# Optimization experiments

Hardware: AMD Instinct MI355X
Metric: run time of the kernel (lower is better)

Reference implementation:

```python
import jax, jax.numpy as jnp
import numpy as np

N, E, T, B, H, V, D = 100000, 400000, 20, 128, 400, 5000, 20


def setup_inputs() -> dict:
    key = jax.random.key(0)
    ks = iter(jax.random.split(key, 64))

    def ri(shape, hi):
        return jax.random.randint(next(ks), shape, 0, hi, dtype=jnp.int32)

    def rn(shape):
        return jax.random.normal(next(ks), shape, dtype=jnp.float32) * 0.05

    inp = {}
    for g in ("pd", "ast", "cf"):
        inp[f"x_{g}"] = ri((N, T), V)            # 20 token ids per node
        inp[f"ei_{g}"] = ri((2, E), N)            # [src; dst]
        inp[f"b_{g}"] = jnp.sort(ri((N,), B))     # graph assignment per node
        inp[f"emb_{g}"] = rn((V, D))
        inp[f"w_{g}"] = rn((3, H, H))             # per-step message weight
        inp[f"wih_{g}"] = rn((H, 3 * H))          # GRUCell input weights (r,z,n)
        inp[f"bih_{g}"] = jnp.zeros((3 * H,), jnp.float32)
        inp[f"whh_{g}"] = rn((H, 3 * H))
        inp[f"bhh_{g}"] = jnp.zeros((3 * H,), jnp.float32)
    for nm, (a, b) in zip(("1", "2", "21", "22", "3", "4"),
                          ((1200, 1000), (1000, 750), (750, 500), (500, 400), (400, 100), (100, 4))):
        inp[f"wl{nm}"] = rn((a, b))
        inp[f"bl{nm}"] = jnp.zeros((b,), jnp.float32)
    return inp


def _gru(m, h, wih, bih, whh, bhh):
    gi = m @ wih + bih
    gh = h @ whh + bhh
    ir, iz, inn = jnp.split(gi, 3, axis=-1)
    hr, hz, hn = jnp.split(gh, 3, axis=-1)
    r = jax.nn.sigmoid(ir + hr)
    z = jax.nn.sigmoid(iz + hz)
    n = jnp.tanh(inn + r * hn)
    return (1.0 - z) * n + z * h


def _ggc(h, ei, w, wih, bih, whh, bhh):
    # GatedGraphConv(H, num_layers=3): message = h @ w[i], scatter-add src->dst, GRU update
    src, dst = ei[0], ei[1]
    n_nodes = h.shape[0]
    for i in range(3):
        m = h @ w[i]                                   # [N, H]
        agg = jax.ops.segment_sum(m[src], dst, num_segments=n_nodes)  # [N, H]
        h = _gru(agg, h, wih, bih, whh, bhh)
    return h


def _branch(x, ei, b, emb, w, wih, bih, whh, bhh):
    h = emb[x].reshape(x.shape[0], -1)                 # [N, T*D] = [N, 400]
    h = jax.nn.relu(_ggc(h, ei, w, wih, bih, whh, bhh))
    pooled = jax.ops.segment_max(h, b, num_segments=B, indices_are_sorted=True)
    return jnp.where(jnp.isfinite(pooled), pooled, 0.0)  # guard empty segments


def reference(x_pd, ei_pd, b_pd, emb_pd, w_pd, wih_pd, bih_pd, whh_pd, bhh_pd,
              x_ast, ei_ast, b_ast, emb_ast, w_ast, wih_ast, bih_ast, whh_ast, bhh_ast,
              x_cf, ei_cf, b_cf, emb_cf, w_cf, wih_cf, bih_cf, whh_cf, bhh_cf,
              wl1, bl1, wl2, bl2, wl21, bl21, wl22, bl22, wl3, bl3, wl4, bl4):
    x1 = _branch(x_pd, ei_pd, b_pd, emb_pd, w_pd, wih_pd, bih_pd, whh_pd, bhh_pd)
    x2 = _branch(x_ast, ei_ast, b_ast, emb_ast, w_ast, wih_ast, bih_ast, whh_ast, bhh_ast)
    x4 = _branch(x_cf, ei_cf, b_cf, emb_cf, w_cf, wih_cf, bih_cf, whh_cf, bhh_cf)
    x = jnp.concatenate([x1, x2, x4], axis=1)          # [B, 1200]
    for wl, bl in ((wl1, bl1), (wl2, bl2), (wl21, bl21), (wl22, bl22), (wl3, bl3), (wl4, bl4)):
        x = jax.nn.relu(x @ wl + bl)                   # dropout inactive in eval mode
    return x
```

## Files before the change

### kernel.cpp

```cpp
#include <hip/hip_runtime.h>

typedef unsigned short u16;
typedef unsigned int u32;
typedef unsigned long long u64;
typedef float f32x4 __attribute__((ext_vector_type(4)));
typedef __bf16 bf16x8 __attribute__((ext_vector_type(8)));

#define KPAD 416
#define SWZ(r) ((((u32)(r)) & 3u) ^ ((((u32)(r)) >> 2) & 3u))

__device__ __forceinline__ float bf2f(u16 v){
  u32 x = ((u32)v) << 16; float f; __builtin_memcpy(&f, &x, 4); return f;
}
__device__ __forceinline__ u16 f2bf(float f){
  u32 x; __builtin_memcpy(&x, &f, 4);
  x += 0x7fffu + ((x >> 16) & 1u);
  return (u16)(x >> 16);
}
__device__ __forceinline__ void gll16(const u16* g, void* l){
  __builtin_amdgcn_global_load_lds(
      (const __attribute__((address_space(1))) u32*)(const void*)g,
      (__attribute__((address_space(3))) u32*)l, 16, 0, 0);
}
__device__ __forceinline__ int xcd_remap(int orig, int nwg){
  int q = nwg >> 3, r = nwg & 7;
  int xcd = orig & 7, idx = orig >> 3;
  return (xcd < r ? xcd * (q + 1) : r * (q + 1) + (xcd - r) * q) + idx;
}

__global__ void embed_k(const int* __restrict__ x, const float* __restrict__ emb,
                        u16* __restrict__ H, int N){
  int tid = blockIdx.x * 256 + threadIdx.x;
  if (tid >= N * 104) return;
  int n = tid / 104, cg = tid % 104, c = cg * 4;
  u16 r0 = 0, r1 = 0, r2 = 0, r3 = 0;
  if (c < 400){
    int t = c / 20, d = c % 20;
    int tok = x[n * 20 + t];
    f32x4 v = *(const f32x4*)(emb + (size_t)tok * 20 + d);
    r0 = f2bf(v[0]); r1 = f2bf(v[1]); r2 = f2bf(v[2]); r3 = f2bf(v[3]);
  }
  u64 pack = (u64)r0 | ((u64)r1 << 16) | ((u64)r2 << 32) | ((u64)r3 << 48);
  *(u64*)(H + (size_t)n * KPAD + c) = pack;
}

__global__ void convw_k(const float* __restrict__ src, u16* __restrict__ dst,
                        int srccols, int nout){
  int tid = blockIdx.x * 256 + threadIdx.x;
  if (tid >= nout * KPAD) return;
  int k = tid % KPAD, n = tid / KPAD;
  dst[tid] = (k < 400) ? f2bf(src[(size_t)k * srccols + n]) : (u16)0;
}

__global__ void pad_w(const float* __restrict__ src, u16* __restrict__ dst, int rows){
  int tid = blockIdx.x * 256 + threadIdx.x;
  if (tid >= rows * KPAD) return;
  int k = tid / KPAD, c = tid % KPAD;
  dst[tid] = (c < 400) ? f2bf(src[(size_t)k * 400 + c]) : (u16)0;
}

__global__ void count_k(const int* __restrict__ ei, int* __restrict__ cnt, int E){
  int t = blockIdx.x * 256 + threadIdx.x; if (t >= E) return;
  atomicAdd(&cnt[ei[E + t] + 1], 1);
}
__global__ void scan_blk(int* __restrict__ data, int* __restrict__ bsum, int total){
  __shared__ int sm[1024];
  int gid = blockIdx.x * 1024 + threadIdx.x;
  sm[threadIdx.x] = (gid < total) ? data[gid] : 0;
  __syncthreads();
  for (int off = 1; off < 1024; off <<= 1){
    int add = (threadIdx.x >= off) ? sm[threadIdx.x - off] : 0;
    __syncthreads();
    sm[threadIdx.x] += add;
    __syncthreads();
  }
  if (gid < total) data[gid] = sm[threadIdx.x];
  if (threadIdx.x == 1023 && bsum) bsum[blockIdx.x] = sm[1023];
}
__global__ void scan_add(int* __restrict__ data, const int* __restrict__ bsum, int total){
  int gid = blockIdx.x * 256 + threadIdx.x;
  if (gid >= total) return;
  int b = gid >> 10;
  if (b > 0) data[gid] += bsum[b - 1];
}
__global__ void copy_k(const int* __restrict__ s, int* __restrict__ d, int n){
  int t = blockIdx.x * 256 + threadIdx.x; if (t < n) d[t] = s[t];
}
__global__ void fill_k(const int* __restrict__ ei, int* __restrict__ cur,
                       int* __restrict__ srcl, int E){
  int t = blockIdx.x * 256 + threadIdx.x; if (t >= E) return;
  int d = ei[E + t];
  int p = atomicAdd(&cur[d], 1);
  srcl[p] = ei[t];
}
__global__ void bound_k(const int* __restrict__ bseg, int* __restrict__ segs, int N){
  int t = threadIdx.x; if (t > 128) return;
  int lo = 0, hi = N;
  while (lo < hi){ int mid = (lo + hi) >> 1; if (bseg[mid] < t) lo = mid + 1; else hi = mid; }
  segs[t] = lo;
}

__global__ void seg_sum(const int* __restrict__ offs, const int* __restrict__ srcl,
                        const u32* __restrict__ Mv, u32* __restrict__ Agg, int N){
  int n = blockIdx.x * 4 + (threadIdx.x >> 6);
  int lane = threadIdx.x & 63;
  if (n >= N || lane >= 52) return;
  int s = offs[n], e = offs[n + 1];
  float a[8] = {0.f,0.f,0.f,0.f,0.f,0.f,0.f,0.f};
  for (int i = s; i < e; i++){
    int sr = srcl[i];
    const u32* p = Mv + (size_t)sr * 208 + lane * 4;
    u32 v0 = p[0], v1 = p[1], v2 = p[2], v3 = p[3];
    a[0] += bf2f((u16)(v0 & 0xffffu)); a[1] += bf2f((u16)(v0 >> 16));
    a[2] += bf2f((u16)(v1 & 0xffffu)); a[3] += bf2f((u16)(v1 >> 16));
    a[4] += bf2f((u16)(v2 & 0xffffu)); a[5] += bf2f((u16)(v2 >> 16));
    a[6] += bf2f((u16)(v3 & 0xffffu)); a[7] += bf2f((u16)(v3 >> 16));
  }
  u32* q = Agg + (size_t)n * 208 + lane * 4;
  q[0] = (u32)f2bf(a[0]) | ((u32)f2bf(a[1]) << 16);
  q[1] = (u32)f2bf(a[2]) | ((u32)f2bf(a[3]) << 16);
  q[2] = (u32)f2bf(a[4]) | ((u32)f2bf(a[5]) << 16);
  q[3] = (u32)f2bf(a[6]) | ((u32)f2bf(a[7]) << 16);
}

__launch_bounds__(256, 2)
__global__ void gemm_msg(const u16* __restrict__ A, const u16* __restrict__ BT,
                         u16* __restrict__ C, int M, int nwg){
  __shared__ __align__(16) u16 smem[2][192 * 32];
  const int tid = threadIdx.x, lane = tid & 63, wave = tid >> 6;
  const int wg = xcd_remap(blockIdx.x, nwg);
  const int m0 = (wg / 7) * 128, n0 = (wg % 7) * 64;

  const u16* gsrc[3]; u32 ldo[3];
#pragma unroll
  for (int i = 0; i < 2; i++){
    u32 o = (u32)(wave * 2 + i) * 1024 + (u32)lane * 16;
    u32 r = o >> 6, cch = (o >> 4) & 3;
    int grow = m0 + (int)r; if (grow > M - 1) grow = M - 1;
    gsrc[i] = A + (size_t)grow * KPAD + ((cch ^ SWZ(r)) << 3);
    ldo[i] = o;
  }
  {
    u32 o = (u32)wave * 1024 + (u32)lane * 16;
    u32 r = o >> 6, cch = (o >> 4) & 3;
    int gn = n0 + (int)r; if (gn > 399) gn = 399;
    gsrc[2] = BT + (size_t)gn * KPAD + ((cch ^ SWZ(r)) << 3);
    ldo[2] = 8192 + o;
  }
  auto stage = [&](int p, int ks){
#pragma unroll
    for (int i = 0; i < 3; i++)
      gll16(gsrc[i] + ks * 32, (char*)smem + (size_t)p * 12288 + ldo[i]);
  };

  const int g = lane >> 4, rl = lane & 15;
  const int ar0 = wave * 32 + rl, ar1 = ar0 + 16;
  const u32 aoff0 = (u32)ar0 * 64 + ((g ^ SWZ(ar0)) << 4);
  const u32 aoff1 = (u32)ar1 * 64 + ((g ^ SWZ(ar1)) << 4);
  u32 boff[4];
#pragma unroll
  for (int j = 0; j < 4; j++){
    int br = j * 16 + rl;
    boff[j] = 8192u + (u32)br * 64 + ((g ^ SWZ(br)) << 4);
  }

  f32x4 zero = {0.f, 0.f, 0.f, 0.f};
  f32x4 acc[2][4];
#pragma unroll
  for (int i = 0; i < 2; i++)
#pragma unroll
    for (int j = 0; j < 4; j++) acc[i][j] = zero;

  stage(0, 0);
  __syncthreads();
  int cur = 0;
  for (int ks = 0; ks < 13; ks++){
    if (ks < 12) stage(cur ^ 1, ks + 1);
    const char* sb = (const char*)smem + (size_t)cur * 12288;
    bf16x8 a0 = *(const bf16x8*)(sb + aoff0);
    bf16x8 a1 = *(const bf16x8*)(sb + aoff1);
#pragma unroll
    for (int j = 0; j < 4; j++){
      bf16x8 bb = *(const bf16x8*)(sb + boff[j]);
      acc[0][j] = __builtin_amdgcn_mfma_f32_16x16x32_bf16(a0, bb, acc[0][j], 0, 0, 0);
      acc[1][j] = __builtin_amdgcn_mfma_f32_16x16x32_bf16(a1, bb, acc[1][j], 0, 0, 0);
    }
    __syncthreads();
    cur ^= 1;
  }

  const int rsub = (lane >> 4) * 4;
#pragma unroll
  for (int i = 0; i < 2; i++){
#pragma unroll
    for (int j = 0; j < 4; j++){
      int col = n0 + j * 16 + rl;
      if (col >= KPAD) continue;
#pragma unroll
      for (int r = 0; r < 4; r++){
        int row = m0 + wave * 32 + i * 16 + rsub + r;
        if (row >= M) continue;
        C[(size_t)row * KPAD + col] = (col < 400) ? f2bf(acc[i][j][r]) : (u16)0;
      }
    }
  }
}

__launch_bounds__(256, 2)
__global__ void gemm_gru(const u16* __restrict__ AG, const u16* __restrict__ AH,
                         const u16* __restrict__ WCT, const u16* __restrict__ WHHT,
                         const float* __restrict__ bih, const float* __restrict__ bhh,
                         u16* __restrict__ Out, int M, int nwg){
  __shared__ __align__(16) u16 lB[2][6144];
  const int tid = threadIdx.x, lane = tid & 63, wave = tid >> 6;
  const int wg = xcd_remap(blockIdx.x, nwg);
  const int m0 = (wg / 13) * 128, c0 = (wg % 13) * 32;

  const u16* gsrcB[3]; u32 ldoB[3];
#pragma unroll
  for (int ii = 0; ii < 3; ii++){
    int id = wave * 3 + ii;
    int tile = id >> 1, half = id & 1;
    const u16* Wsrc = (tile < 3) ? WCT : WHHT;
    int s = (tile < 3) ? tile : tile - 3;
    u32 o = (u32)half * 1024 + (u32)lane * 16;
    u32 r = o >> 6, cch = (o >> 4) & 3;
    int ncol = c0 + (int)r; if (ncol > 399) ncol = 399;
    gsrcB[ii] = Wsrc + (size_t)(s * 400 + ncol) * KPAD + ((cch ^ SWZ(r)) << 3);
    ldoB[ii] = (u32)tile * 2048 + o;
  }
  auto stageB = [&](int p, int ks){
#pragma unroll
    for (int ii = 0; ii < 3; ii++)
      gll16(gsrcB[ii] + ks * 32, (char*)(&lB[0][0]) + (size_t)p * 12288 + ldoB[ii]);
  };

  const int g = lane >> 4, rl = lane & 15;
  int rr0 = m0 + wave * 32 + rl;      if (rr0 > M - 1) rr0 = M - 1;
  int rr1 = m0 + wave * 32 + 16 + rl; if (rr1 > M - 1) rr1 = M - 1;
  const u16* pAG0 = AG + (size_t)rr0 * KPAD + g * 8;
  const u16* pAG1 = AG + (size_t)rr1 * KPAD + g * 8;
  const u16* pAH0 = AH + (size_t)rr0 * KPAD + g * 8;
  const u16* pAH1 = AH + (size_t)rr1 * KPAD + g * 8;

  u32 boffj[2];
#pragma unroll
  for (int j = 0; j < 2; j++){
    int br = j * 16 + rl;
    boffj[j] = (u32)br * 64 + ((g ^ SWZ(br)) << 4);
  }

  f32x4 zero = {0.f, 0.f, 0.f, 0.f};
  f32x4 acc[6][2][2];
#pragma unroll
  for (int t = 0; t < 6; t++)
#pragma unroll
    for (int i = 0; i < 2; i++)
#pragma unroll
      for (int j = 0; j < 2; j++) acc[t][i][j] = zero;

  bf16x8 aX[4], aY[4];
  auto loadA = [&](bf16x8 (&d)[4], int ks){
    d[0] = *(const bf16x8*)(pAG0 + ks * 32);
    d[1] = *(const bf16x8*)(pAG1 + ks * 32);
    d[2] = *(const bf16x8*)(pAH0 + ks * 32);
    d[3] = *(const bf16x8*)(pAH1 + ks * 32);
  };
  int cur = 0;
  auto body = [&](bf16x8 (&ac)[4], bf16x8 (&an)[4], int ks){
    if (ks < 12){ loadA(an, ks + 1); stageB(cur ^ 1, ks + 1); }
    const char* sb = (const char*)(&lB[0][0]) + (size_t)cur * 12288;
#pragma unroll
    for (int t = 0; t < 6; t++){
      bf16x8 b0 = *(const bf16x8*)(sb + t * 2048 + boffj[0]);
      bf16x8 b1 = *(const bf16x8*)(sb + t * 2048 + boffj[1]);
      bf16x8 x0 = (t < 3) ? ac[0] : ac[2];
      bf16x8 x1 = (t < 3) ? ac[1] : ac[3];
      acc[t][0][0] = __builtin_amdgcn_mfma_f32_16x16x32_bf16(x0, b0, acc[t][0][0], 0, 0, 0);
      acc[t][0][1] = __builtin_amdgcn_mfma_f32_16x16x32_bf16(x0, b1, acc[t][0][1], 0, 0, 0);
      acc[t][1][0] = __builtin_amdgcn_mfma_f32_16x16x32_bf16(x1, b0, acc[t][1][0], 0, 0, 0);
      acc[t][1][1] = __builtin_amdgcn_mfma_f32_16x16x32_bf16(x1, b1, acc[t][1][1], 0, 0, 0);
    }
    __syncthreads();
    cur ^= 1;
  };
  loadA(aX, 0);
  stageB(0, 0);
  __syncthreads();
#pragma unroll
  for (int kk = 0; kk < 6; kk++){
    body(aX, aY, 2 * kk);
    body(aY, aX, 2 * kk + 1);
  }
  body(aX, aY, 12);

  const int rsub = (lane >> 4) * 4;
#pragma unroll
  for (int j = 0; j < 2; j++){
    int col = c0 + j * 16 + rl;
    bool valid = col < 400;
    float bir = 0, biz = 0, bin = 0, bhr = 0, bhz = 0, bhn = 0;
    if (valid){
      bir = bih[col]; biz = bih[400 + col]; bin = bih[800 + col];
      bhr = bhh[col]; bhz = bhh[400 + col]; bhn = bhh[800 + col];
    }
#pragma unroll
    for (int i = 0; i < 2; i++){
#pragma unroll
      for (int r = 0; r < 4; r++){
        int row = m0 + wave * 32 + i * 16 + rsub + r;
        if (row >= M) continue;
        u16 outv = 0;
        if (valid){
          float ir = acc[0][i][j][r] + bir, iz = acc[1][i][j][r] + biz, inn = acc[2][i][j][r] + bin;
          float hr = acc[3][i][j][r] + bhr, hz = acc[4][i][j][r] + bhz, hn = acc[5][i][j][r] + bhn;
          float rg = 1.f / (1.f + __expf(-(ir + hr)));
          float zg = 1.f / (1.f + __expf(-(iz + hz)));
          float nx = inn + rg * hn;
          float tn = 1.f - 2.f / (1.f + __expf(2.f * nx));
          float hp = bf2f(AH[(size_t)row * KPAD + col]);
          float hv = (1.f - zg) * tn + zg * hp;
          outv = f2bf(hv);
        }
        Out[(size_t)row * KPAD + col] = outv;
      }
    }
  }
}

__global__ void pool_max(const u16* __restrict__ H, const int* __restrict__ segs,
                         u32* __restrict__ pooled, int goff){
  int b = blockIdx.x;
  int c = blockIdx.y * 256 + threadIdx.x;
  if (c >= 400) return;
  int s = segs[b], e = segs[b + 1], len = e - s;
  int chunk = blockIdx.z;
  int cs = s + (int)((long long)len * chunk / 4);
  int ce = s + (int)((long long)len * (chunk + 1) / 4);
  float mx = 0.f;
  for (int n = cs; n < ce; n++) mx = fmaxf(mx, bf2f(H[(size_t)n * KPAD + c]));
  if (mx > 0.f){
    u32 bits; __builtin_memcpy(&bits, &mx, 4);
    atomicMax(&pooled[b * 1200 + goff + c], bits);
  }
}

__global__ void wt_k(const float* __restrict__ src, float* __restrict__ dst,
                     int K, int Nout){
  int t = blockIdx.x * 256 + threadIdx.x;
  if (t >= K * Nout) return;
  int n = t / K, k = t % K;
  dst[t] = src[(size_t)k * Nout + n];
}
__global__ void mlp_dot(const float* __restrict__ A, const float* __restrict__ WT,
                        const float* __restrict__ bias, float* __restrict__ out,
                        int K, int Nout){
  int gw = (int)((blockIdx.x * 256u + threadIdx.x) >> 6);
  int lane = threadIdx.x & 63;
  if (gw >= 128 * Nout) return;
  int m = gw / Nout, n = gw % Nout;
  const float* a = A + (size_t)m * K;
  const float* w = WT + (size_t)n * K;
  float acc = 0.f;
  for (int k = lane; k < K; k += 64) acc = fmaf(a[k], w[k], acc);
#pragma unroll
  for (int off = 32; off; off >>= 1) acc += __shfl_xor(acc, off);
  if (lane == 0) out[(size_t)m * Nout + n] = fmaxf(acc + bias[n], 0.f);
}

extern "C" void kernel_launch(void* const* d_in, const int* in_sizes, int n_in,
                              void* d_out, int out_size, void* d_ws, size_t ws_size,
                              hipStream_t stream){
  const int N = in_sizes[2];
  const int E = in_sizes[1] / 2;

  char* base = (char*)d_ws;
  size_t off = 0;
  auto alloc = [&](size_t sz) -> char* {
    char* r = base + off;
    off += (sz + 255) & ~(size_t)255;
    return r;
  };
  u16* hA    = (u16*)alloc((size_t)N * KPAD * 2);
  u16* hB    = (u16*)alloc((size_t)N * KPAD * 2);
  u16* hC    = (u16*)alloc((size_t)N * KPAD * 2);
  u16* wcT   = (u16*)alloc((size_t)3 * 1200 * KPAD * 2);
  u16* whhT  = (u16*)alloc((size_t)1200 * KPAD * 2);
  u16* wihT  = (u16*)alloc((size_t)1200 * KPAD * 2);
  u16* wPad  = (u16*)alloc((size_t)3 * 400 * KPAD * 2);
  float* pooled = (float*)alloc((size_t)128 * 1200 * 4);
  float* mAb = (float*)alloc((size_t)128 * 1000 * 4);
  float* mBb = (float*)alloc((size_t)128 * 1000 * 4);
  float* wtb = (float*)alloc((size_t)1200 * 1000 * 4);
  int* offs  = (int*)alloc((size_t)(N + 1) * 4);
  int* cur   = (int*)alloc((size_t)N * 4);
  int* srcl  = (int*)alloc((size_t)E * 4);
  int* bsum  = (int*)alloc(4096);
  int* segs  = (int*)alloc(1024);
  if (off > ws_size) return;

  const int NB = (N + 1 + 1023) / 1024;
  const int MT = (N + 127) / 128;
  const int nwg_gru = MT * 13;
  const int MT_f = (1200 + 127) / 128;
  const int nwg_f = MT_f * 7;

  hipMemsetAsync(pooled, 0, (size_t)128 * 1200 * 4, stream);

  for (int g = 0; g < 3; g++){
    const int*   x    = (const int*)  d_in[g * 9 + 0];
    const int*   ei   = (const int*)  d_in[g * 9 + 1];
    const int*   bseg = (const int*)  d_in[g * 9 + 2];
    const float* emb  = (const float*)d_in[g * 9 + 3];
    const float* w    = (const float*)d_in[g * 9 + 4];
    const float* wih  = (const float*)d_in[g * 9 + 5];
    const float* bihp = (const float*)d_in[g * 9 + 6];
    const float* whh  = (const float*)d_in[g * 9 + 7];
    const float* bhhp = (const float*)d_in[g * 9 + 8];

    hipMemsetAsync(offs, 0, (size_t)(N + 1) * 4, stream);
    count_k<<<(E + 255) / 256, 256, 0, stream>>>(ei, offs, E);
    scan_blk<<<NB, 1024, 0, stream>>>(offs, bsum, N + 1);
    scan_blk<<<1, 1024, 0, stream>>>(bsum, (int*)nullptr, NB);
    scan_add<<<(N + 1 + 255) / 256, 256, 0, stream>>>(offs, bsum, N + 1);
    copy_k<<<(N + 255) / 256, 256, 0, stream>>>(offs, cur, N);
    fill_k<<<(E + 255) / 256, 256, 0, stream>>>(ei, cur, srcl, E);
    bound_k<<<1, 256, 0, stream>>>(bseg, segs, N);

    convw_k<<<(1200 * KPAD + 255) / 256, 256, 0, stream>>>(whh, whhT, 1200, 1200);
    convw_k<<<(1200 * KPAD + 255) / 256, 256, 0, stream>>>(wih, wihT, 1200, 1200);
    pad_w<<<(3 * 400 * KPAD + 255) / 256, 256, 0, stream>>>(w, wPad, 3 * 400);
    for (int l = 0; l < 3; l++)
      gemm_msg<<<nwg_f, 256, 0, stream>>>(wihT, wPad + (size_t)l * 400 * KPAD,
                                          wcT + (size_t)l * 1200 * KPAD, 1200, nwg_f);

    embed_k<<<(N * 104 + 255) / 256, 256, 0, stream>>>(x, emb, hA, N);

    u16* hcur = hA; u16* hoth = hB;
    for (int l = 0; l < 3; l++){
      seg_sum<<<(N + 3) / 4, 256, 0, stream>>>(offs, srcl, (const u32*)hcur, (u32*)hC, N);
      gemm_gru<<<nwg_gru, 256, 0, stream>>>(hC, hcur, wcT + (size_t)l * 1200 * KPAD,
                                            whhT, bihp, bhhp, hoth, N, nwg_gru);
      u16* t = hcur; hcur = hoth; hoth = t;
    }
    pool_max<<<dim3(128, 2, 4), 256, 0, stream>>>(hcur, segs, (u32*)pooled, g * 400);
  }

  const float* wl[6] = {(const float*)d_in[27], (const float*)d_in[29], (const float*)d_in[31],
                        (const float*)d_in[33], (const float*)d_in[35], (const float*)d_in[37]};
  const float* bl[6] = {(const float*)d_in[28], (const float*)d_in[30], (const float*)d_in[32],
                        (const float*)d_in[34], (const float*)d_in[36], (const float*)d_in[38]};
  int dims[7] = {1200, 1000, 750, 500, 400, 100, 4};
  const float* cin = pooled;
  for (int li = 0; li < 6; li++){
    int K = dims[li], Nout = dims[li + 1];
    wt_k<<<(K * Nout + 255) / 256, 256, 0, stream>>>(wl[li], wtb, K, Nout);
    float* cout = (li == 5) ? (float*)d_out : (((li & 1) == 0) ? mAb : mBb);
    int waves = 128 * Nout;
    mlp_dot<<<(waves + 3) / 4, 256, 0, stream>>>(cin, wtb, bl[li], cout, K, Nout);
    cin = cout;
  }
}
```

Baseline: 4.016 ms.

## Triple-buffer GRU GEMM weight staging and batch message-weight folding launches

```diff
diff --git a/kernel.cpp b/kernel.cpp
--- a/kernel.cpp
+++ b/kernel.cpp
@@ -124,11 +124,14 @@
 }
 
 __launch_bounds__(256, 2)
-__global__ void gemm_msg(const u16* __restrict__ A, const u16* __restrict__ BT,
-                         u16* __restrict__ C, int M, int nwg){
+__global__ void gemm_msg(const u16* __restrict__ A, const u16* __restrict__ BT0,
+                         u16* __restrict__ C0, int M, int nwg, int nfold){
   __shared__ __align__(16) u16 smem[2][192 * 32];
   const int tid = threadIdx.x, lane = tid & 63, wave = tid >> 6;
-  const int wg = xcd_remap(blockIdx.x, nwg);
+  const int wgall = xcd_remap(blockIdx.x, nwg * nfold);
+  const int fold = wgall / nwg, wg = wgall % nwg;
+  const u16* BT = BT0 + (size_t)fold * 400 * KPAD;
+  u16* C = C0 + (size_t)fold * 1200 * KPAD;
   const int m0 = (wg / 7) * 128, n0 = (wg % 7) * 64;
 
   const u16* gsrc[3]; u32 ldo[3];
@@ -211,7 +214,7 @@
                          const u16* __restrict__ WCT, const u16* __restrict__ WHHT,
                          const float* __restrict__ bih, const float* __restrict__ bhh,
                          u16* __restrict__ Out, int M, int nwg){
-  __shared__ __align__(16) u16 lB[2][6144];
+  __shared__ __align__(16) u16 lB[3][6144];
   const int tid = threadIdx.x, lane = tid & 63, wave = tid >> 6;
   const int wg = xcd_remap(blockIdx.x, nwg);
   const int m0 = (wg / 13) * 128, c0 = (wg % 13) * 32;
@@ -266,10 +269,15 @@
     d[2] = *(const bf16x8*)(pAH0 + ks * 32);
     d[3] = *(const bf16x8*)(pAH1 + ks * 32);
   };
-  int cur = 0;
-  auto body = [&](bf16x8 (&ac)[4], bf16x8 (&an)[4], int ks){
-    if (ks < 12){ loadA(an, ks + 1); stageB(cur ^ 1, ks + 1); }
-    const char* sb = (const char*)(&lB[0][0]) + (size_t)cur * 12288;
+
+  auto body = [&](bf16x8 (&ac)[4], bf16x8 (&an)[4], int k){
+    asm volatile("s_waitcnt vmcnt(7)" ::: "memory");
+    __builtin_amdgcn_s_barrier();
+    __builtin_amdgcn_sched_barrier(0);
+    if (k + 2 <= 12) stageB((k + 2) % 3, k + 2);
+    if (k + 1 <= 12) loadA(an, k + 1);
+    const char* sb = (const char*)(&lB[0][0]) + (size_t)(k % 3) * 12288;
+    __builtin_amdgcn_s_setprio(1);
 #pragma unroll
     for (int t = 0; t < 6; t++){
       bf16x8 b0 = *(const bf16x8*)(sb + t * 2048 + boffj[0]);
@@ -281,17 +289,17 @@
       acc[t][1][0] = __builtin_amdgcn_mfma_f32_16x16x32_bf16(x1, b0, acc[t][1][0], 0, 0, 0);
       acc[t][1][1] = __builtin_amdgcn_mfma_f32_16x16x32_bf16(x1, b1, acc[t][1][1], 0, 0, 0);
     }
-    __syncthreads();
-    cur ^= 1;
+    __builtin_amdgcn_s_setprio(0);
   };
+
+  stageB(0, 0);
+  asm volatile("" ::: "memory");
   loadA(aX, 0);
-  stageB(0, 0);
-  __syncthreads();
-#pragma unroll
-  for (int kk = 0; kk < 6; kk++){
-    body(aX, aY, 2 * kk);
-    body(aY, aX, 2 * kk + 1);
-  }
+  stageB(1, 1);
+
+  body(aX, aY, 0);  body(aY, aX, 1);  body(aX, aY, 2);  body(aY, aX, 3);
+  body(aX, aY, 4);  body(aY, aX, 5);  body(aX, aY, 6);  body(aY, aX, 7);
+  body(aX, aY, 8);  body(aY, aX, 9);  body(aX, aY, 10); body(aY, aX, 11);
   body(aX, aY, 12);
 
   const int rsub = (lane >> 4) * 4;
@@ -430,9 +438,7 @@
     convw_k<<<(1200 * KPAD + 255) / 256, 256, 0, stream>>>(whh, whhT, 1200, 1200);
     convw_k<<<(1200 * KPAD + 255) / 256, 256, 0, stream>>>(wih, wihT, 1200, 1200);
     pad_w<<<(3 * 400 * KPAD + 255) / 256, 256, 0, stream>>>(w, wPad, 3 * 400);
-    for (int l = 0; l < 3; l++)
-      gemm_msg<<<nwg_f, 256, 0, stream>>>(wihT, wPad + (size_t)l * 400 * KPAD,
-                                          wcT + (size_t)l * 1200 * KPAD, 1200, nwg_f);
+    gemm_msg<<<nwg_f * 3, 256, 0, stream>>>(wihT, wPad, wcT, 1200, nwg_f, 3);
 
     embed_k<<<(N * 104 + 255) / 256, 256, 0, stream>>>(x, emb, hA, N);
 
```

Result: no change. 3.955 ms (-1.5%).
